# Optimization experiments

Hardware: AMD Instinct MI355X
Metric: run time of the kernel (lower is better)

The kernel has to match this reference:

```python
import jax, jax.numpy as jnp
import numpy as np

H = 8          # num_channels (heads)
POS = 16       # pos_dim
MAX_F = 16.0
MIN_F = 1.0
HALF_S = 16    # samples_per_dim=32 -> offsets -16..16, S=33
SCALE = POS ** -0.5


def setup_inputs() -> dict:
    key = jax.random.key(0)
    ks = jax.random.split(key, 12)
    B, L, C = 2, 4096, 1024
    p = 0.02
    return {
        'x': jax.random.normal(ks[0], (B, L, C), jnp.float32),
        'wave_w': jax.random.normal(ks[1], (C, 3 * H), jnp.float32) * p,
        'wave_b': jax.random.normal(ks[2], (3 * H,), jnp.float32) * p,
        'query_w': jax.random.normal(ks[3], (C, H * POS), jnp.float32) * p,
        'query_b': jax.random.normal(ks[4], (H * POS,), jnp.float32) * p,
        'key_w': jax.random.normal(ks[5], (POS,), jnp.float32) * p,
        'out_w': jax.random.normal(ks[6], (C, C), jnp.float32) * p,
        'se1_w': jax.random.normal(ks[7], (C, C // 4), jnp.float32) * p,
        'se1_b': jax.random.normal(ks[8], (C // 4,), jnp.float32) * p,
        'se2_w': jax.random.normal(ks[9], (C // 4, C), jnp.float32) * p,
        'se2_b': jax.random.normal(ks[10], (C,), jnp.float32) * p,
    }


def _adaptive_conv(x, wave_w, wave_b, query_w, query_b, key_w, out_w,
                   se1_w, se1_b, se2_w, se2_b):
    B, L, C = x.shape
    D = C // H
    silu = jax.nn.silu
    offsets = jnp.arange(-HALF_S, HALF_S + 1, dtype=x.dtype)  # [S]
    S = offsets.shape[0]

    # wave params -> freq/phase/decay per (B,L,H)
    wave = silu(x @ wave_w + wave_b).reshape(B, L, 3, H)
    freq = jax.nn.sigmoid(wave[:, :, 0, :]) * (MAX_F - MIN_F) + MIN_F
    phase = jnp.tanh(wave[:, :, 1, :]) * MAX_F
    decay = jax.nn.sigmoid(wave[:, :, 2, :]) * 9.5 + 0.5
    queries = silu(x @ query_w + query_b).reshape(B, L, H, POS)

    freq_avg = freq.mean(axis=-1)    # [B,L]
    phase_avg = phase.mean(axis=-1)  # [B,L]

    centers = jnp.arange(L, dtype=x.dtype)
    # [B,L,S] real-valued sample positions
    sample_pos = (centers[None, :, None]
                  + offsets[None, None, :] * freq_avg[..., None]
                  + phase_avg[..., None])
    valid = (sample_pos >= 0) & (sample_pos < L)           # [B,L,S]
    sample_idx = jnp.clip(sample_pos.astype(jnp.int32), 0, L - 1)

    # gather: values[b,l,s,:] = x[b, sample_idx[b,l,s], :]
    values = jnp.take_along_axis(x, sample_idx.reshape(B, L * S, 1), axis=1)
    values = values.reshape(B, L, S, H, D).transpose(0, 1, 3, 2, 4)  # [B,L,H,S,D]

    rel = jnp.abs(offsets)[None, None, None, :] * freq[..., None]    # [B,L,H,S]
    keys = silu(rel[..., None] * key_w)                              # [B,L,H,S,POS]
    logits = jnp.einsum('blhd,blhsd->blhs', queries, keys) * SCALE

    vmask = valid[:, :, None, :]                                     # [B,L,H,S]
    logits = jnp.where(vmask, logits, -1e30)
    env = jnp.exp(-rel / jnp.maximum(decay[..., None], 0.1))
    w = jax.nn.softmax(logits, axis=-1) * env * vmask.astype(x.dtype)
    w = w / (w.sum(axis=-1, keepdims=True) + 1e-8)

    out = jnp.einsum('blhsd,blhs->blhd', values, w).reshape(B, L, C)
    se = jax.nn.sigmoid(silu(out @ se1_w + se1_b) @ se2_w + se2_b)
    out = out * se
    return silu(out @ out_w)


def reference(x, wave_w, wave_b, query_w, query_b, key_w, out_w,
              se1_w, se1_b, se2_w, se2_b):
    return _adaptive_conv(x, wave_w, wave_b, query_w, query_b, key_w,
                          out_w, se1_w, se1_b, se2_w, se2_b)
```

## Files before the change

### kernel.cpp

```cpp
#include <hip/hip_runtime.h>
#include <math.h>

#define HN 8
#define POSN 16
#define SN 33
#define HALF_SN 16
#define CDIM 1024
#define LDIM 4096
#define BDIM 2
#define NTOK (BDIM * LDIM)

typedef unsigned short u16;
typedef short short8 __attribute__((ext_vector_type(8)));
typedef u16 u16x8 __attribute__((ext_vector_type(8)));
typedef unsigned int u32x4 __attribute__((ext_vector_type(4)));
typedef float f32x4 __attribute__((ext_vector_type(4)));

__device__ __forceinline__ float sigf(float x) { return 1.0f / (1.0f + expf(-x)); }
__device__ __forceinline__ float siluf(float x) { return x / (1.0f + expf(-x)); }
__device__ __forceinline__ float frcp(float x) { return __builtin_amdgcn_rcpf(x); }
__device__ __forceinline__ float fexp(float x) { return __expf(x); }
__device__ __forceinline__ float fsig(float x) { return frcp(1.0f + fexp(-x)); }
__device__ __forceinline__ float fsilu(float x) { return x * fsig(x); }

__device__ __forceinline__ u16 f2b(float f) {
    union { float f; unsigned u; } v; v.f = f;
    unsigned r = v.u + 0x7fffu + ((v.u >> 16) & 1u);
    return (u16)(r >> 16);
}
__device__ __forceinline__ float b2f(u16 v) {
    union { unsigned u; float f; } x; x.u = ((unsigned)v) << 16; return x.f;
}
__device__ __forceinline__ float u2f(unsigned u) {
    union { unsigned u; float f; } x; x.u = u; return x.f;
}
__device__ __forceinline__ void ld_lds16(const void* g, void* l) {
    __builtin_amdgcn_global_load_lds(
        (const __attribute__((address_space(1))) void*)g,
        (__attribute__((address_space(3))) void*)l, 16, 0, 0);
}

__global__ __launch_bounds__(256) void transcast_all(
    const float* __restrict__ qw, const float* __restrict__ s1,
    const float* __restrict__ s2, const float* __restrict__ ow,
    u16* __restrict__ oq, u16* __restrict__ o1,
    u16* __restrict__ o2, u16* __restrict__ oo)
{
    const int bid = blockIdx.x;
    const float* in; u16* out; int N, K, base;
    if      (bid < 128) { in = qw; out = oq; N = 128;  K = 1024; base = 0;   }
    else if (bid < 384) { in = s1; out = o1; N = 256;  K = 1024; base = 128; }
    else if (bid < 640) { in = s2; out = o2; N = 1024; K = 256;  base = 384; }
    else                { in = ow; out = oo; N = 1024; K = 1024; base = 640; }
    const int rel = bid - base, nx = N / 32;
    const int bn = (rel % nx) * 32, bk = (rel / nx) * 32;

    __shared__ float tile[32][33];
    const int tx = threadIdx.x & 31, ty = threadIdx.x >> 5;
    #pragma unroll
    for (int yy = ty; yy < 32; yy += 8)
        tile[yy][tx] = in[(size_t)(bk + yy) * N + bn + tx];
    __syncthreads();
    #pragma unroll
    for (int yy = ty; yy < 32; yy += 8)
        out[(size_t)(bn + yy) * K + bk + tx] = f2b(tile[tx][yy]);
}

__global__ __launch_bounds__(256) void wave_kernel(
    const float* __restrict__ x, const float* __restrict__ wave_w,
    const float* __restrict__ wave_b, u16* __restrict__ xbf,
    float* __restrict__ freq, float* __restrict__ decay,
    float* __restrict__ favg, float* __restrict__ pavg)
{
    const int tid = threadIdx.x;
    const int tok = tid >> 5, col = tid & 31;
    const int t0 = blockIdx.x * 8;
    const int t = t0 + tok;
    __shared__ float wsct[24][260];
    __shared__ float wsh[8][24];
    __shared__ float fsh[8][8], psh[8][8];

    for (int i = tid; i < 1024; i += 256) {
        const int r = i >> 7, c8 = (i & 127) * 8;
        const float* src = x + (size_t)(t0 + r) * CDIM + c8;
        float4 a = *(const float4*)(src);
        float4 b = *(const float4*)(src + 4);
        u16x8 o;
        o[0]=f2b(a.x); o[1]=f2b(a.y); o[2]=f2b(a.z); o[3]=f2b(a.w);
        o[4]=f2b(b.x); o[5]=f2b(b.y); o[6]=f2b(b.z); o[7]=f2b(b.w);
        *(u16x8*)(xbf + (size_t)(t0 + r) * CDIM + c8) = o;
    }

    const float* xrow = x + (size_t)t * CDIM;
    float acc = (col < 24) ? wave_b[col] : 0.0f;

    for (int k0 = 0; k0 < CDIM; k0 += 256) {
        __syncthreads();
        {
            const float* wr = wave_w + (size_t)(k0 + tid) * 24;
            float4 w0 = *(const float4*)(wr + 0);
            float4 w1 = *(const float4*)(wr + 4);
            float4 w2 = *(const float4*)(wr + 8);
            float4 w3 = *(const float4*)(wr + 12);
            float4 w4 = *(const float4*)(wr + 16);
            float4 w5 = *(const float4*)(wr + 20);
            wsct[0][tid]=w0.x;  wsct[1][tid]=w0.y;  wsct[2][tid]=w0.z;  wsct[3][tid]=w0.w;
            wsct[4][tid]=w1.x;  wsct[5][tid]=w1.y;  wsct[6][tid]=w1.z;  wsct[7][tid]=w1.w;
            wsct[8][tid]=w2.x;  wsct[9][tid]=w2.y;  wsct[10][tid]=w2.z; wsct[11][tid]=w2.w;
            wsct[12][tid]=w3.x; wsct[13][tid]=w3.y; wsct[14][tid]=w3.z; wsct[15][tid]=w3.w;
            wsct[16][tid]=w4.x; wsct[17][tid]=w4.y; wsct[18][tid]=w4.z; wsct[19][tid]=w4.w;
            wsct[20][tid]=w5.x; wsct[21][tid]=w5.y; wsct[22][tid]=w5.z; wsct[23][tid]=w5.w;
        }
        __syncthreads();
        if (col < 24) {
            #pragma unroll 4
            for (int kk = 0; kk < 256; kk += 4) {
                float4 xv = *(const float4*)(xrow + k0 + kk);
                float4 wv = *(const float4*)(&wsct[col][kk]);
                acc += xv.x * wv.x; acc += xv.y * wv.y;
                acc += xv.z * wv.z; acc += xv.w * wv.w;
            }
        }
    }
    if (col < 24) wsh[tok][col] = siluf(acc);
    __syncthreads();
    if (col < 8) {
        float f = sigf(wsh[tok][col])      * 15.0f + 1.0f;
        float p = tanhf(wsh[tok][8 + col]) * 16.0f;
        float d = sigf(wsh[tok][16 + col]) * 9.5f + 0.5f;
        freq[(size_t)t * HN + col] = f;
        decay[(size_t)t * HN + col] = d;
        fsh[tok][col] = f; psh[tok][col] = p;
    }
    __syncthreads();
    if (col == 0) {
        float fa = 0.f, pa = 0.f;
        for (int h = 0; h < HN; ++h) { fa += fsh[tok][h]; pa += psh[tok][h]; }
        favg[t] = fa * 0.125f; pavg[t] = pa * 0.125f;
    }
}

template <int MODE, int CFG>
__global__ __launch_bounds__(256) void mfma_gemm(
    const u16* __restrict__ A, const u16* __restrict__ Bt,
    const float* __restrict__ bias, const u16* __restrict__ mulb,
    void* __restrict__ Cptr, int M, int N, int K)
{
    constexpr int BM  = (CFG == 0) ? 128 : 32;
    constexpr int MI  = (CFG == 0) ? 4 : 2;
    constexpr int NJ  = (CFG == 0) ? 4 : 2;
    constexpr int ACH = BM / 16;
    constexpr int NCH = ACH + 8;

    __shared__ u16 lds[2][(BM + 128) * 32];

    const int nwg = gridDim.x * gridDim.y;
    const int flat = blockIdx.y * gridDim.x + blockIdx.x;
    const int swz = (flat & 7) * (nwg >> 3) + (flat >> 3);
    const int bxi = swz / gridDim.y, byi = swz % gridDim.y;

    const int tid = threadIdx.x;
    const int bm = bxi * BM, bn = byi * 128;
    const int wid = tid >> 6, lane = tid & 63;
    const int wr = (CFG == 0) ? (wid >> 1) * 64 : 0;
    const int wc = (CFG == 0) ? (wid & 1) * 64 : wid * 32;
    const int fm = lane & 15;
    const int kg = (lane >> 4) * 8;
    const int lrow = lane >> 2;
    const int lk   = (lane & 3) * 8;

    f32x4 acc[MI][NJ];
    #pragma unroll
    for (int i = 0; i < MI; ++i)
        #pragma unroll
        for (int j = 0; j < NJ; ++j) acc[i][j] = (f32x4){0.f, 0.f, 0.f, 0.f};

    auto stage = [&](u16* dst, int k0s) {
        #pragma unroll
        for (int c = wid; c < NCH; c += 4) {
            const u16* gsrc = (c < ACH)
                ? A  + (size_t)(bm + c * 16 + lrow) * K + k0s + lk
                : Bt + (size_t)(bn + (c - ACH) * 16 + lrow) * K + k0s + lk;
            ld_lds16(gsrc, dst + c * 512 + lane * 8);
        }
    };

    stage(&lds[0][0], 0);
    __syncthreads();
    int cur = 0;
    for (int k0 = 0; k0 < K; k0 += 32) {
        const int k1 = (k0 + 32 < K) ? (k0 + 32) : k0;
        stage(&lds[cur ^ 1][0], k1);
        short8 a[MI], b[NJ];
        #pragma unroll
        for (int i = 0; i < MI; ++i)
            a[i] = *(const short8*)&lds[cur][(wr + i * 16 + fm) * 32 + kg];
        #pragma unroll
        for (int j = 0; j < NJ; ++j)
            b[j] = *(const short8*)&lds[cur][(BM + wc + j * 16 + fm) * 32 + kg];
        #pragma unroll
        for (int i = 0; i < MI; ++i)
            #pragma unroll
            for (int j = 0; j < NJ; ++j)
                acc[i][j] = __builtin_amdgcn_mfma_f32_16x16x32_bf16(a[i], b[j], acc[i][j], 0, 0, 0);
        __syncthreads();
        cur ^= 1;
    }

    float* Cf = (float*)Cptr;
    u16* Cb = (u16*)Cptr;
    #pragma unroll
    for (int i = 0; i < MI; ++i) {
        const int row0 = bm + wr + i * 16 + (lane >> 4) * 4;
        #pragma unroll
        for (int j = 0; j < NJ; ++j) {
            const int col = bn + wc + j * 16 + fm;
            const float vb = (MODE == 3) ? 0.0f : bias[col];
            #pragma unroll
            for (int e = 0; e < 4; ++e) {
                const int row = row0 + e;
                float v = acc[i][j][e];
                if (MODE == 1) v = fsilu(v + vb);
                if (MODE == 2) v = fsig(v + vb) * b2f(mulb[(size_t)row * N + col]);
                if (MODE == 3) v = fsilu(v);
                if (MODE == 3) Cf[(size_t)row * N + col] = v;
                else           Cb[(size_t)row * N + col] = f2b(v);
            }
        }
    }
}

__global__ __launch_bounds__(256) void adaptconv_kernel(
    const u16* __restrict__ xbf, const float* __restrict__ key_w,
    const u16* __restrict__ qb, const float* __restrict__ freq,
    const float* __restrict__ decay, const float* __restrict__ favg,
    const float* __restrict__ pavg, u16* __restrict__ out)
{
    const int bid = blockIdx.x;
    const int swz = (bid & 7) * (NTOK / 16) + (bid >> 3);
    const int sub = threadIdx.x >> 7, lt = threadIdx.x & 127;
    const int t = swz * 2 + sub;
    const int b = t / LDIM, l = t % LDIM;
    const int h = lt >> 4;
    const int li = lt & 15;

    __shared__ float qs[2][HN][17];
    __shared__ float kw[POSN];
    __shared__ float fr[2][HN], dc[2][HN];
    __shared__ int   boff[2][SN];
    __shared__ float msk[2][SN];
    __shared__ float vsh[2][HN][17];
    __shared__ float esh[2][HN][17];
    __shared__ float wgt[2][HN][SN];

    qs[sub][lt >> 4][lt & 15] = b2f(qb[(size_t)t * 128 + lt]);
    if (threadIdx.x < POSN) kw[threadIdx.x] = key_w[threadIdx.x];
    if (lt < HN) {
        fr[sub][lt] = freq[(size_t)t * HN + lt];
        dc[sub][lt] = decay[(size_t)t * HN + lt];
    }
    if (lt < SN) {
        float fa = favg[t], pa = pavg[t];
        float sp = (float)l + (float)(lt - HALF_SN) * fa + pa;
        bool v = (sp >= 0.0f) && (sp < (float)LDIM);
        int si = (int)sp;
        si = min(max(si, 0), LDIM - 1);
        boff[sub][lt] = si * (CDIM * 2);
        msk[sub][lt] = v ? 1.0f : 0.0f;
    }
    __syncthreads();

    {
        const float fh = fr[sub][h];
        const float rdci = frcp(fmaxf(dc[sub][h], 0.1f));
        for (int ds = li; ds < 17; ds += 16) {
            float rel = (float)ds * fh;
            float acc = 0.0f;
            #pragma unroll
            for (int p = 0; p < POSN; ++p)
                acc += qs[sub][h][p] * fsilu(rel * kw[p]);
            vsh[sub][h][ds] = 0.25f * acc;
            esh[sub][h][ds] = fexp(-rel * rdci);
        }
    }
    __syncthreads();

    {
        const int ns = (li == 0) ? 3 : 2;
        int   sI[3] = { li, li + 16, 32 };
        float lg[3];
        #pragma unroll
        for (int k = 0; k < 3; ++k) {
            if (k < ns) {
                const int s = sI[k], ds = abs(s - 16);
                lg[k] = (msk[sub][s] != 0.0f) ? vsh[sub][h][ds] : -1e30f;
            } else lg[k] = -3.4e38f;
        }
        float m = fmaxf(lg[0], fmaxf(lg[1], lg[2]));
        #pragma unroll
        for (int d = 1; d < 16; d <<= 1) m = fmaxf(m, __shfl_xor(m, d));

        float e[3]; float ssum = 0.0f;
        #pragma unroll
        for (int k = 0; k < 3; ++k) {
            e[k] = (k < ns) ? fexp(lg[k] - m) : 0.0f;
            ssum += e[k];
        }
        #pragma unroll
        for (int d = 1; d < 16; d <<= 1) ssum += __shfl_xor(ssum, d);

        const float rss = frcp(ssum);
        float wv[3]; float wsum = 0.0f;
        #pragma unroll
        for (int k = 0; k < 3; ++k) {
            if (k < ns) {
                const int s = sI[k], ds = abs(s - 16);
                wv[k] = e[k] * rss * esh[sub][h][ds] * msk[sub][s];
            } else wv[k] = 0.0f;
            wsum += wv[k];
        }
        #pragma unroll
        for (int d = 1; d < 16; d <<= 1) wsum += __shfl_xor(wsum, d);

        const float inv = frcp(wsum + 1e-8f);
        #pragma unroll
        for (int k = 0; k < 3; ++k)
            if (k < ns) wgt[sub][h][sI[k]] = wv[k] * inv;
    }
    __syncthreads();

    const char* xbB = (const char*)(xbf + (size_t)b * LDIM * CDIM);
    const int cbyte = lt * 16;
    float a0=0,a1=0,a2=0,a3=0,a4=0,a5=0,a6=0,a7=0;

    #define GFMA(V, W) do { \
        a0 += (W) * u2f((V)[0] << 16); a1 += (W) * u2f((V)[0] & 0xffff0000u); \
        a2 += (W) * u2f((V)[1] << 16); a3 += (W) * u2f((V)[1] & 0xffff0000u); \
        a4 += (W) * u2f((V)[2] << 16); a5 += (W) * u2f((V)[2] & 0xffff0000u); \
        a6 += (W) * u2f((V)[3] << 16); a7 += (W) * u2f((V)[3] & 0xffff0000u); } while (0)

    int s = 0;
    for (; s + 4 <= SN; s += 4) {
        u32x4 v0 = *(const u32x4*)(xbB + boff[sub][s]     + cbyte);
        u32x4 v1 = *(const u32x4*)(xbB + boff[sub][s + 1] + cbyte);
        u32x4 v2 = *(const u32x4*)(xbB + boff[sub][s + 2] + cbyte);
        u32x4 v3 = *(const u32x4*)(xbB + boff[sub][s + 3] + cbyte);
        float w0 = wgt[sub][h][s],     w1 = wgt[sub][h][s + 1];
        float w2 = wgt[sub][h][s + 2], w3 = wgt[sub][h][s + 3];
        GFMA(v0, w0); GFMA(v1, w1); GFMA(v2, w2); GFMA(v3, w3);
    }
    for (; s < SN; ++s) {
        u32x4 v = *(const u32x4*)(xbB + boff[sub][s] + cbyte);
        float w = wgt[sub][h][s];
        GFMA(v, w);
    }
    #undef GFMA

    u16x8 o;
    o[0]=f2b(a0); o[1]=f2b(a1); o[2]=f2b(a2); o[3]=f2b(a3);
    o[4]=f2b(a4); o[5]=f2b(a5); o[6]=f2b(a6); o[7]=f2b(a7);
    *(u16x8*)(out + (size_t)t * CDIM + lt * 8) = o;
}

extern "C" void kernel_launch(void* const* d_in, const int* in_sizes, int n_in,
                              void* d_out, int out_size, void* d_ws, size_t ws_size,
                              hipStream_t stream)
{
    const float* x       = (const float*)d_in[0];
    const float* wave_w  = (const float*)d_in[1];
    const float* wave_b  = (const float*)d_in[2];
    const float* query_w = (const float*)d_in[3];
    const float* query_b = (const float*)d_in[4];
    const float* key_w   = (const float*)d_in[5];
    const float* out_w   = (const float*)d_in[6];
    const float* se1_w   = (const float*)d_in[7];
    const float* se1_b   = (const float*)d_in[8];
    const float* se2_w   = (const float*)d_in[9];
    const float* se2_b   = (const float*)d_in[10];

    char* wsb = (char*)d_ws;
    u16* q_bf    = (u16*)wsb;           wsb += (size_t)NTOK * 128 * 2;
    float* freq  = (float*)wsb;         wsb += (size_t)NTOK * HN * 4;
    float* decay = (float*)wsb;         wsb += (size_t)NTOK * HN * 4;
    float* favg  = (float*)wsb;         wsb += (size_t)NTOK * 4;
    float* pavg  = (float*)wsb;         wsb += (size_t)NTOK * 4;
    u16* x_bf    = (u16*)wsb;           wsb += (size_t)NTOK * CDIM * 2;
    u16* conv_bf = (u16*)wsb;           wsb += (size_t)NTOK * CDIM * 2;
    u16* tmp1_bf = (u16*)wsb;           wsb += (size_t)NTOK * 256 * 2;
    u16* g_bf    = (u16*)wsb;           wsb += (size_t)NTOK * CDIM * 2;
    u16* qw_bf   = (u16*)wsb;           wsb += (size_t)128 * CDIM * 2;
    u16* se1w_bf = (u16*)wsb;           wsb += (size_t)256 * CDIM * 2;
    u16* se2w_bf = (u16*)wsb;           wsb += (size_t)CDIM * 256 * 2;
    u16* outw_bf = (u16*)wsb;           wsb += (size_t)CDIM * CDIM * 2;

    transcast_all<<<1664, 256, 0, stream>>>(
        query_w, se1_w, se2_w, out_w, qw_bf, se1w_bf, se2w_bf, outw_bf);

    wave_kernel<<<NTOK / 8, 256, 0, stream>>>(
        x, wave_w, wave_b, x_bf, freq, decay, favg, pavg);

    mfma_gemm<1, 1><<<dim3(NTOK / 32, 1), 256, 0, stream>>>(
        x_bf, qw_bf, query_b, nullptr, q_bf, NTOK, 128, CDIM);

    adaptconv_kernel<<<NTOK / 2, 256, 0, stream>>>(
        x_bf, key_w, q_bf, freq, decay, favg, pavg, conv_bf);

    mfma_gemm<1, 1><<<dim3(NTOK / 32, 256 / 128), 256, 0, stream>>>(
        conv_bf, se1w_bf, se1_b, nullptr, tmp1_bf, NTOK, 256, CDIM);

    mfma_gemm<2, 0><<<dim3(NTOK / 128, CDIM / 128), 256, 0, stream>>>(
        tmp1_bf, se2w_bf, se2_b, conv_bf, g_bf, NTOK, CDIM, 256);

    mfma_gemm<3, 0><<<dim3(NTOK / 128, CDIM / 128), 256, 0, stream>>>(
        g_bf, outw_bf, nullptr, nullptr, d_out, NTOK, CDIM, CDIM);
}
```

Before: 145.7 us.

## Pre-transpose wave weights and compute three wave outputs per thread without LDS

```diff
diff --git a/kernel.cpp b/kernel.cpp
--- a/kernel.cpp
+++ b/kernel.cpp
@@ -43,10 +43,18 @@
 __global__ __launch_bounds__(256) void transcast_all(
     const float* __restrict__ qw, const float* __restrict__ s1,
     const float* __restrict__ s2, const float* __restrict__ ow,
+    const float* __restrict__ ww,
     u16* __restrict__ oq, u16* __restrict__ o1,
-    u16* __restrict__ o2, u16* __restrict__ oo)
+    u16* __restrict__ o2, u16* __restrict__ oo,
+    float* __restrict__ owT)
 {
     const int bid = blockIdx.x;
+    if (bid >= 1664) {
+        const int idx = (bid - 1664) * 256 + threadIdx.x;
+        const int c = idx >> 10, k = idx & 1023;
+        owT[idx] = ww[k * 24 + c];
+        return;
+    }
     const float* in; u16* out; int N, K, base;
     if      (bid < 128) { in = qw; out = oq; N = 128;  K = 1024; base = 0;   }
     else if (bid < 384) { in = s1; out = o1; N = 256;  K = 1024; base = 128; }
@@ -66,21 +74,20 @@
         out[(size_t)(bn + yy) * K + bk + tx] = f2b(tile[tx][yy]);
 }
 
-__global__ __launch_bounds__(256) void wave_kernel(
-    const float* __restrict__ x, const float* __restrict__ wave_w,
+__global__ __launch_bounds__(128) void wave_kernel(
+    const float* __restrict__ x, const float* __restrict__ wwT,
     const float* __restrict__ wave_b, u16* __restrict__ xbf,
     float* __restrict__ freq, float* __restrict__ decay,
     float* __restrict__ favg, float* __restrict__ pavg)
 {
     const int tid = threadIdx.x;
-    const int tok = tid >> 5, col = tid & 31;
-    const int t0 = blockIdx.x * 8;
-    const int t = t0 + tok;
-    __shared__ float wsct[24][260];
-    __shared__ float wsh[8][24];
-    __shared__ float fsh[8][8], psh[8][8];
-
-    for (int i = tid; i < 1024; i += 256) {
+    const int tok = tid >> 3;
+    const int cg  = tid & 7;
+    const int t0 = blockIdx.x * 16;
+    const int t  = t0 + tok;
+    __shared__ float fsh[16][9], psh[16][9];
+
+    for (int i = tid; i < 2048; i += 128) {
         const int r = i >> 7, c8 = (i & 127) * 8;
         const float* src = x + (size_t)(t0 + r) * CDIM + c8;
         float4 a = *(const float4*)(src);
@@ -92,48 +99,33 @@
     }
 
     const float* xrow = x + (size_t)t * CDIM;
-    float acc = (col < 24) ? wave_b[col] : 0.0f;
-
-    for (int k0 = 0; k0 < CDIM; k0 += 256) {
-        __syncthreads();
-        {
-            const float* wr = wave_w + (size_t)(k0 + tid) * 24;
-            float4 w0 = *(const float4*)(wr + 0);
-            float4 w1 = *(const float4*)(wr + 4);
-            float4 w2 = *(const float4*)(wr + 8);
-            float4 w3 = *(const float4*)(wr + 12);
-            float4 w4 = *(const float4*)(wr + 16);
-            float4 w5 = *(const float4*)(wr + 20);
-            wsct[0][tid]=w0.x;  wsct[1][tid]=w0.y;  wsct[2][tid]=w0.z;  wsct[3][tid]=w0.w;
-            wsct[4][tid]=w1.x;  wsct[5][tid]=w1.y;  wsct[6][tid]=w1.z;  wsct[7][tid]=w1.w;
-            wsct[8][tid]=w2.x;  wsct[9][tid]=w2.y;  wsct[10][tid]=w2.z; wsct[11][tid]=w2.w;
-            wsct[12][tid]=w3.x; wsct[13][tid]=w3.y; wsct[14][tid]=w3.z; wsct[15][tid]=w3.w;
-            wsct[16][tid]=w4.x; wsct[17][tid]=w4.y; wsct[18][tid]=w4.z; wsct[19][tid]=w4.w;
-            wsct[20][tid]=w5.x; wsct[21][tid]=w5.y; wsct[22][tid]=w5.z; wsct[23][tid]=w5.w;
-        }
-        __syncthreads();
-        if (col < 24) {
-            #pragma unroll 4
-            for (int kk = 0; kk < 256; kk += 4) {
-                float4 xv = *(const float4*)(xrow + k0 + kk);
-                float4 wv = *(const float4*)(&wsct[col][kk]);
-                acc += xv.x * wv.x; acc += xv.y * wv.y;
-                acc += xv.z * wv.z; acc += xv.w * wv.w;
-            }
-        }
-    }
-    if (col < 24) wsh[tok][col] = siluf(acc);
-    __syncthreads();
-    if (col < 8) {
-        float f = sigf(wsh[tok][col])      * 15.0f + 1.0f;
-        float p = tanhf(wsh[tok][8 + col]) * 16.0f;
-        float d = sigf(wsh[tok][16 + col]) * 9.5f + 0.5f;
-        freq[(size_t)t * HN + col] = f;
-        decay[(size_t)t * HN + col] = d;
-        fsh[tok][col] = f; psh[tok][col] = p;
-    }
-    __syncthreads();
-    if (col == 0) {
+    const float* wT0 = wwT + (size_t)cg * 1024;
+    const float* wT1 = wwT + (size_t)(8 + cg) * 1024;
+    const float* wT2 = wwT + (size_t)(16 + cg) * 1024;
+    float acc0 = wave_b[cg];
+    float acc1 = wave_b[8 + cg];
+    float acc2 = wave_b[16 + cg];
+
+    #pragma unroll 4
+    for (int kk = 0; kk < CDIM; kk += 4) {
+        float4 xv = *(const float4*)(xrow + kk);
+        float4 w0 = *(const float4*)(wT0 + kk);
+        float4 w1 = *(const float4*)(wT1 + kk);
+        float4 w2 = *(const float4*)(wT2 + kk);
+        acc0 += xv.x * w0.x; acc1 += xv.x * w1.x; acc2 += xv.x * w2.x;
+        acc0 += xv.y * w0.y; acc1 += xv.y * w1.y; acc2 += xv.y * w2.y;
+        acc0 += xv.z * w0.z; acc1 += xv.z * w1.z; acc2 += xv.z * w2.z;
+        acc0 += xv.w * w0.w; acc1 += xv.w * w1.w; acc2 += xv.w * w2.w;
+    }
+
+    float f = sigf(siluf(acc0)) * 15.0f + 1.0f;
+    float p = tanhf(siluf(acc1)) * 16.0f;
+    float d = sigf(siluf(acc2)) * 9.5f + 0.5f;
+    freq[(size_t)t * HN + cg] = f;
+    decay[(size_t)t * HN + cg] = d;
+    fsh[tok][cg] = f; psh[tok][cg] = p;
+    __syncthreads();
+    if (cg == 0) {
         float fa = 0.f, pa = 0.f;
         for (int h = 0; h < HN; ++h) { fa += fsh[tok][h]; pa += psh[tok][h]; }
         favg[t] = fa * 0.125f; pavg[t] = pa * 0.125f;
@@ -392,12 +384,14 @@
     u16* se1w_bf = (u16*)wsb;           wsb += (size_t)256 * CDIM * 2;
     u16* se2w_bf = (u16*)wsb;           wsb += (size_t)CDIM * 256 * 2;
     u16* outw_bf = (u16*)wsb;           wsb += (size_t)CDIM * CDIM * 2;
-
-    transcast_all<<<1664, 256, 0, stream>>>(
-        query_w, se1_w, se2_w, out_w, qw_bf, se1w_bf, se2w_bf, outw_bf);
-
-    wave_kernel<<<NTOK / 8, 256, 0, stream>>>(
-        x, wave_w, wave_b, x_bf, freq, decay, favg, pavg);
+    float* wwT   = (float*)wsb;         wsb += (size_t)24 * CDIM * 4;
+
+    transcast_all<<<1760, 256, 0, stream>>>(
+        query_w, se1_w, se2_w, out_w, wave_w,
+        qw_bf, se1w_bf, se2w_bf, outw_bf, wwT);
+
+    wave_kernel<<<NTOK / 16, 128, 0, stream>>>(
+        x, wwT, wave_b, x_bf, freq, decay, favg, pavg);
 
     mfma_gemm<1, 1><<<dim3(NTOK / 32, 1), 256, 0, stream>>>(
         x_bf, qw_bf, query_b, nullptr, q_bf, NTOK, 128, CDIM);
```

Measured after the change: 204.3 us. +40.2%, slower.
